# Kernel tuning notes

Measured on AMD Instinct MI355X. Metric: run time of the kernel, lower is better.

## Reference

```python
import jax, jax.numpy as jnp
import numpy as np
from jax import lax

ALPHA = 0.98
DELTA = 2.0
R = 0.5
S = 0.025
EPS = 1e-6


def setup_inputs() -> dict:
    key = jax.random.key(0)
    # non-negative energy spectrogram [B, n_mels, T]
    x = jax.random.uniform(key, (64, 128, 4000), dtype=jnp.float32)
    return {"x": x}


def _pcen(x):
    # x: [B, C, T]; EMA smoother: smooth[0] = x[0], smooth[t] = (1-s)*smooth[t-1] + s*x[t]
    xt = jnp.moveaxis(x, -1, 0)  # [T, B, C]

    def step(carry, x_t):
        sm = (1.0 - S) * carry + S * x_t
        return sm, sm

    init = xt[0]
    _, sm_rest = lax.scan(step, init, xt[1:])  # [T-1, B, C]
    smooth = jnp.concatenate([init[None], sm_rest], axis=0)  # [T, B, C]
    smooth = jnp.moveaxis(smooth, 0, -1)  # [B, C, T]
    pcen = (x / (smooth + EPS) ** ALPHA + DELTA) ** R - DELTA ** R
    return pcen


def reference(x):
    return _pcen(x)
```

## Files before the change

kernel.cpp:

```cpp
#include <hip/hip_runtime.h>
#include <math.h>


constexpr int   TLEN = 4000;
constexpr int   NF4  = 1000;
constexpr int   NTH  = 256;
constexpr float S_C  = 0.025f;
constexpr float A_1  = 1.0f - S_C;

constexpr float fpow(float b, int n) {
    float r = 1.0f;
    for (int i = 0; i < n; ++i) r *= b;
    return r;
}
constexpr float A_2  = fpow(A_1, 2);
constexpr float A_3  = fpow(A_1, 3);
constexpr float A256 = fpow(A_1, 256);

constexpr float L2A4 = -0.14610359f;

constexpr float ALPHA = 0.98f;
constexpr float EPS_C = 1e-6f;
constexpr float SQRT2 = 1.41421356237309515f;

__device__ __forceinline__ float pcen_elem(float x, float sm) {
    float t = sm + EPS_C;
    float p = __builtin_amdgcn_exp2f(-ALPHA * __builtin_amdgcn_logf(t));
    float y = fmaf(x, p, 2.0f);
    return __builtin_amdgcn_sqrtf(y) - SQRT2;
}

__global__ __launch_bounds__(NTH) void pcen_kernel(const float* __restrict__ x,
                                                   float* __restrict__ out) {
    const int    tid  = threadIdx.x;
    const int    lane = tid & 63;
    const int    wv   = tid >> 6;
    const size_t base = (size_t)blockIdx.x * TLEN;

    const float4* __restrict__ x4 = (const float4*)(x + base);
    float4*       __restrict__ o4 = (float4*)(out + base);

    float4 v[4];
    bool   act[4];
#pragma unroll
    for (int k = 0; k < 4; ++k) {
        int f4 = tid + NTH * k;
        act[k] = (f4 < NF4);
        v[k]   = act[k] ? x4[f4] : make_float4(0.f, 0.f, 0.f, 0.f);
    }

    float B[4];
#pragma unroll
    for (int k = 0; k < 4; ++k) {
        float4 r  = v[k];
        float  b0 = (tid == 0 && k == 0) ? r.x : S_C * r.x;
        B[k] = fmaf(A_3, b0, S_C * fmaf(A_2, r.y, fmaf(A_1, r.z, r.w)));
    }

    constexpr float CD[6] = { fpow(A_1, 4),  fpow(A_1, 8),   fpow(A_1, 16),
                              fpow(A_1, 32), fpow(A_1, 64),  fpow(A_1, 128) };
#pragma unroll
    for (int s = 0; s < 6; ++s) {
        const int   d = 1 << s;
        const float c = CD[s];
        float Bp[4];
#pragma unroll
        for (int k = 0; k < 4; ++k) Bp[k] = __shfl_up(B[k], d);
        const bool ok = (lane >= d);
#pragma unroll
        for (int k = 0; k < 4; ++k) B[k] = fmaf(c, ok ? Bp[k] : 0.0f, B[k]);
    }

    __shared__ float sB[16];
    if (lane == 63) {
#pragma unroll
        for (int k = 0; k < 4; ++k) sB[4 * k + wv] = B[k];
    }
    __syncthreads();

    float E0, E1, E2, E3;
    {
        float e = 0.0f;
#define CH(m) e = fmaf(A256, e, sB[m]);
        if (wv == 0) {
            E0 = e;
            CH(0) CH(1) CH(2)  E1 = fmaf(A256, e, sB[3]);  CH(3)
            CH(4) CH(5) CH(6)  E2 = fmaf(A256, e, sB[7]);  CH(7)
            CH(8) CH(9) CH(10) E3 = fmaf(A256, e, sB[11]);
        } else if (wv == 1) {
            CH(0)  E0 = e;
            CH(1) CH(2) CH(3)  CH(4)  E1 = e;
            CH(5) CH(6) CH(7)  CH(8)  E2 = e;
            CH(9) CH(10) CH(11) CH(12) E3 = e;
        } else if (wv == 2) {
            CH(0) CH(1)  E0 = e;
            CH(2) CH(3) CH(4) CH(5)   E1 = e;
            CH(6) CH(7) CH(8) CH(9)   E2 = e;
            CH(10) CH(11) CH(12) CH(13) E3 = e;
        } else {
            CH(0) CH(1) CH(2)  E0 = e;
            CH(3) CH(4) CH(5) CH(6)   E1 = e;
            CH(7) CH(8) CH(9) CH(10)  E2 = e;
            CH(11) CH(12) CH(13) CH(14) E3 = e;
        }
#undef CH
    }
    const float E[4] = { E0, E1, E2, E3 };

    const float Al = __builtin_amdgcn_exp2f((float)lane * L2A4);

#pragma unroll
    for (int k = 0; k < 4; ++k) {
        float Bi = __shfl_up(B[k], 1);
        if (lane == 0) Bi = 0.0f;
        float sm = fmaf(Al, E[k], Bi);

        float4 r  = v[k];
        float  b0 = (tid == 0 && k == 0) ? r.x : S_C * r.x;
        float  s0 = fmaf(A_1, sm, b0);
        float  s1 = fmaf(A_1, s0, S_C * r.y);
        float  s2 = fmaf(A_1, s1, S_C * r.z);
        float  s3 = fmaf(A_1, s2, S_C * r.w);

        float4 o;
        o.x = pcen_elem(r.x, s0);
        o.y = pcen_elem(r.y, s1);
        o.z = pcen_elem(r.z, s2);
        o.w = pcen_elem(r.w, s3);

        int f4 = tid + NTH * k;
        if (act[k]) o4[f4] = o;
    }
}

extern "C" void kernel_launch(void* const* d_in, const int* in_sizes, int n_in,
                              void* d_out, int out_size, void* d_ws, size_t ws_size,
                              hipStream_t stream) {
    const float* x   = (const float*)d_in[0];
    float*       out = (float*)d_out;
    const int nch    = in_sizes[0] / TLEN;
    pcen_kernel<<<nch, NTH, 0, stream>>>(x, out);
}
```

Baseline: 226.0 us.

## Assign one wavefront per channel and chain chunk carries in registers

Each 64-lane wavefront now processes a whole channel of 4000 samples, holding 16 float4 per lane, instead of a 256-thread block splitting each channel. The cross-wave carry through shared memory and __syncthreads is replaced by a serial register recurrence that broadcasts lane 63 of each chunk. This removes block-level synchronisation and LDS traffic but raises register pressure (64 floats of input plus 16 partial sums) and adds a serial dependency across the 16 chunks, which may lower occupancy.

```diff
diff --git a/kernel.cpp b/kernel.cpp
--- a/kernel.cpp
+++ b/kernel.cpp
@@ -5,6 +5,7 @@
 constexpr int   TLEN = 4000;
 constexpr int   NF4  = 1000;
 constexpr int   NTH  = 256;
+constexpr int   KPL  = 16;
 constexpr float S_C  = 0.025f;
 constexpr float A_1  = 1.0f - S_C;
 
@@ -31,92 +32,58 @@
 }
 
 __global__ __launch_bounds__(NTH) void pcen_kernel(const float* __restrict__ x,
-                                                   float* __restrict__ out) {
-    const int    tid  = threadIdx.x;
-    const int    lane = tid & 63;
-    const int    wv   = tid >> 6;
-    const size_t base = (size_t)blockIdx.x * TLEN;
+                                                   float* __restrict__ out,
+                                                   int nch) {
+    const int lane = threadIdx.x & 63;
+    const int ch   = blockIdx.x * (NTH / 64) + (threadIdx.x >> 6);
+    if (ch >= nch) return;
 
+    const size_t base = (size_t)ch * TLEN;
     const float4* __restrict__ x4 = (const float4*)(x + base);
     float4*       __restrict__ o4 = (float4*)(out + base);
 
-    float4 v[4];
-    bool   act[4];
+    float4 v[KPL];
 #pragma unroll
-    for (int k = 0; k < 4; ++k) {
-        int f4 = tid + NTH * k;
-        act[k] = (f4 < NF4);
-        v[k]   = act[k] ? x4[f4] : make_float4(0.f, 0.f, 0.f, 0.f);
+    for (int k = 0; k < KPL; ++k) {
+        int f4 = lane + 64 * k;
+        v[k] = (f4 < NF4) ? x4[f4] : make_float4(0.f, 0.f, 0.f, 0.f);
     }
 
-    float B[4];
+    float B[KPL];
 #pragma unroll
-    for (int k = 0; k < 4; ++k) {
+    for (int k = 0; k < KPL; ++k) {
         float4 r  = v[k];
-        float  b0 = (tid == 0 && k == 0) ? r.x : S_C * r.x;
+        float  b0 = (lane == 0 && k == 0) ? r.x : S_C * r.x;
         B[k] = fmaf(A_3, b0, S_C * fmaf(A_2, r.y, fmaf(A_1, r.z, r.w)));
     }
 
-    constexpr float CD[6] = { fpow(A_1, 4),  fpow(A_1, 8),   fpow(A_1, 16),
-                              fpow(A_1, 32), fpow(A_1, 64),  fpow(A_1, 128) };
+    constexpr float CD[6] = { fpow(A_1, 4),  fpow(A_1, 8),  fpow(A_1, 16),
+                              fpow(A_1, 32), fpow(A_1, 64), fpow(A_1, 128) };
 #pragma unroll
     for (int s = 0; s < 6; ++s) {
-        const int   d = 1 << s;
-        const float c = CD[s];
-        float Bp[4];
+        const int   d  = 1 << s;
+        const float cc = CD[s];
+        float Bp[KPL];
 #pragma unroll
-        for (int k = 0; k < 4; ++k) Bp[k] = __shfl_up(B[k], d);
+        for (int k = 0; k < KPL; ++k) Bp[k] = __shfl_up(B[k], d);
         const bool ok = (lane >= d);
 #pragma unroll
-        for (int k = 0; k < 4; ++k) B[k] = fmaf(c, ok ? Bp[k] : 0.0f, B[k]);
+        for (int k = 0; k < KPL; ++k)
+            B[k] = fmaf(cc, ok ? Bp[k] : 0.0f, B[k]);
     }
-
-    __shared__ float sB[16];
-    if (lane == 63) {
-#pragma unroll
-        for (int k = 0; k < 4; ++k) sB[4 * k + wv] = B[k];
-    }
-    __syncthreads();
-
-    float E0, E1, E2, E3;
-    {
-        float e = 0.0f;
-#define CH(m) e = fmaf(A256, e, sB[m]);
-        if (wv == 0) {
-            E0 = e;
-            CH(0) CH(1) CH(2)  E1 = fmaf(A256, e, sB[3]);  CH(3)
-            CH(4) CH(5) CH(6)  E2 = fmaf(A256, e, sB[7]);  CH(7)
-            CH(8) CH(9) CH(10) E3 = fmaf(A256, e, sB[11]);
-        } else if (wv == 1) {
-            CH(0)  E0 = e;
-            CH(1) CH(2) CH(3)  CH(4)  E1 = e;
-            CH(5) CH(6) CH(7)  CH(8)  E2 = e;
-            CH(9) CH(10) CH(11) CH(12) E3 = e;
-        } else if (wv == 2) {
-            CH(0) CH(1)  E0 = e;
-            CH(2) CH(3) CH(4) CH(5)   E1 = e;
-            CH(6) CH(7) CH(8) CH(9)   E2 = e;
-            CH(10) CH(11) CH(12) CH(13) E3 = e;
-        } else {
-            CH(0) CH(1) CH(2)  E0 = e;
-            CH(3) CH(4) CH(5) CH(6)   E1 = e;
-            CH(7) CH(8) CH(9) CH(10)  E2 = e;
-            CH(11) CH(12) CH(13) CH(14) E3 = e;
-        }
-#undef CH
-    }
-    const float E[4] = { E0, E1, E2, E3 };
 
     const float Al = __builtin_amdgcn_exp2f((float)lane * L2A4);
 
+    float e = 0.0f;
 #pragma unroll
-    for (int k = 0; k < 4; ++k) {
+    for (int k = 0; k < KPL; ++k) {
+        float Tk = (k < KPL - 1) ? __shfl(B[k], 63) : 0.0f;
         float Bi = __shfl_up(B[k], 1);
         if (lane == 0) Bi = 0.0f;
-        float sm = fmaf(Al, E[k], Bi);
+        float sm = fmaf(Al, e, Bi);
 
         float4 r  = v[k];
-        float  b0 = (tid == 0 && k == 0) ? r.x : S_C * r.x;
+        float  b0 = (lane == 0 && k == 0) ? r.x : S_C * r.x;
         float  s0 = fmaf(A_1, sm, b0);
         float  s1 = fmaf(A_1, s0, S_C * r.y);
         float  s2 = fmaf(A_1, s1, S_C * r.z);
@@ -128,8 +95,10 @@
         o.z = pcen_elem(r.z, s2);
         o.w = pcen_elem(r.w, s3);
 
-        int f4 = tid + NTH * k;
-        if (act[k]) o4[f4] = o;
+        int f4 = lane + 64 * k;
+        if (f4 < NF4) o4[f4] = o;
+
+        e = fmaf(A256, e, Tk);
     }
 }
 
@@ -139,5 +108,7 @@
     const float* x   = (const float*)d_in[0];
     float*       out = (float*)d_out;
     const int nch    = in_sizes[0] / TLEN;
-    pcen_kernel<<<nch, NTH, 0, stream>>>(x, out);
+    const int wpb    = NTH / 64;
+    const int grid   = (nch + wpb - 1) / wpb;
+    pcen_kernel<<<grid, NTH, 0, stream>>>(x, out, nch);
 }
```

Result: no change. 228.3 us (+1.1%).
